# Kernel optimization log

Measured on AMD Instinct MI355X. Metric: run time of the kernel, lower is better.

## Reference

```python
import jax, jax.numpy as jnp
import numpy as np
from jax.scipy.special import logsumexp

D = 256            # descriptor_dim == output_dim
H = 4              # attention heads (hard-coded in AttentionalGNN)
DH = D // H        # 64 per-head dim
KNN = 20           # k for dynamic kNN graph
N_LAYERS = 18      # ['self','cross'] * 9
SINKHORN_ITERS = 20
MATCH_THRESHOLD = 0.2
BN_EPS = 1e-5
N_KPTS = 1024
B = 1
KENC_CH = [D + 4, D // 4, D // 2, D, 2 * D, D]


def conv1(x, w, b):
    # kernel-size-1 Conv1d: x [B,Cin,N], w [Cout,Cin], b [Cout]
    return jnp.einsum('oc,bcn->bon', w, x) + b[:, None]


def bn(x, g, be):
    # training-mode BatchNorm1d over (batch, length), biased variance
    m = jnp.mean(x, axis=(0, 2), keepdims=True)
    v = jnp.var(x, axis=(0, 2), keepdims=True)
    return g[:, None] * (x - m) * jax.lax.rsqrt(v + BN_EPS) + be[:, None]


def run_kenc(desc, kpts, sc, ws, bs, gs, bes):
    # desc [B,N,D], kpts [B,N,3], sc [B,N] -> [B,D,N]
    x = jnp.concatenate([jnp.swapaxes(desc, 1, 2), jnp.swapaxes(kpts, 1, 2), sc[:, None, :]], axis=1)
    for i in range(4):
        x = jax.nn.relu(bn(conv1(x, ws[i], bs[i]), gs[i], bes[i]))
    return conv1(x, ws[4], bs[4])


def run_chebconv(x, pos, cw, cb):
    # x [1,D,N], pos [1,N,3]; dynamic kNN graph + ChebConv K=3, aggr='add'
    p = pos[0]
    n = p.shape[0]
    g = p @ p.T
    sq = jnp.diagonal(g)
    d = sq[:, None] + sq[None, :] - 2.0 * g           # squared pairwise dist [N,N]
    d = d.at[jnp.arange(n), jnp.arange(n)].set(jnp.inf)  # no self-loops
    _, nbr = jax.lax.top_k(-d, KNN)                   # [N,KNN] neighbor indices
    src = jnp.repeat(jnp.arange(n), KNN)              # query node of each edge
    dst = nbr.reshape(-1)                             # neighbor (message target)
    h = x[0].T                                        # [N,D]
    def prop(t):
        # scaled Laplacian propagation: L_hat edge weight = -1/k (self-loops cancel)
        return jnp.zeros_like(t).at[dst].add(t[src]) * (-1.0 / KNN)
    tx0 = h
    tx1 = prop(tx0)
    tx2 = 2.0 * prop(tx1) - tx0
    out = tx0 @ cw[0].T + tx1 @ cw[1].T + tx2 @ cw[2].T + cb
    return out.T[None]                                # [1,D,N]


def attn_prop(x, src, pw, pb, mw, mb, m1w, m1b, g, be, m2w, m2b):
    # AttentionalPropagation: MHA(x, src, src) then MLP([2D,2D,D]) on concat
    b, _, n = x.shape
    m = src.shape[2]
    q = conv1(x, pw[0], pb[0]).reshape(b, DH, H, n)
    k = conv1(src, pw[1], pb[1]).reshape(b, DH, H, m)
    v = conv1(src, pw[2], pb[2]).reshape(b, DH, H, m)
    scores = jnp.einsum('bdhn,bdhm->bhnm', q, k) / (DH ** 0.5)
    prob = jax.nn.softmax(scores, axis=-1)
    msg = jnp.einsum('bhnm,bdhm->bdhn', prob, v).reshape(b, D, n)
    msg = conv1(msg, mw, mb)
    y = jnp.concatenate([x, msg], axis=1)
    y = jax.nn.relu(bn(conv1(y, m1w, m1b), g, be))
    return conv1(y, m2w, m2b)


def log_optimal_transport(scores, alpha, iters):
    b, m, n = scores.shape
    bins0 = jnp.broadcast_to(alpha, (b, m, 1)).astype(scores.dtype)
    bins1 = jnp.broadcast_to(alpha, (b, 1, n)).astype(scores.dtype)
    binsa = jnp.broadcast_to(alpha, (b, 1, 1)).astype(scores.dtype)
    Z = jnp.concatenate([jnp.concatenate([scores, bins0], 2), jnp.concatenate([bins1, binsa], 2)], 1)
    norm = -np.log(float(m + n))
    log_mu = jnp.concatenate([jnp.full((m,), norm, scores.dtype), jnp.asarray([np.log(float(n)) + norm], scores.dtype)])
    log_nu = jnp.concatenate([jnp.full((n,), norm, scores.dtype), jnp.asarray([np.log(float(m)) + norm], scores.dtype)])
    log_mu = jnp.broadcast_to(log_mu[None], (b, m + 1))
    log_nu = jnp.broadcast_to(log_nu[None], (b, n + 1))
    def step(uv, _):
        u, v = uv
        u = log_mu - logsumexp(Z + v[:, None, :], axis=2)
        v = log_nu - logsumexp(Z + u[:, :, None], axis=1)
        return (u, v), None
    (u, v), _ = jax.lax.scan(step, (jnp.zeros_like(log_mu), jnp.zeros_like(log_nu)), None, length=iters)
    return Z + u[:, :, None] + v[:, None, :] - norm


def _forward(h1, h2, uc1, uc2, sc1, sc2, kws, kbs, kgs, kbes, cheb_w, cheb_b,
             gpw, gpb, gmw, gmb, g1w, g1b, gg, gbe, g2w, g2b, fp_w, fp_b, bin_score):
    d1 = run_kenc(h1, uc1, sc1, kws, kbs, kgs, kbes)
    d2 = run_kenc(h2, uc2, sc2, kws, kbs, kgs, kbes)
    d1 = run_chebconv(d1, uc1, cheb_w, cheb_b)
    d2 = run_chebconv(d2, uc2, cheb_w, cheb_b)
    for i in range(N_LAYERS):
        cross = (i % 2 == 1)
        s0, s1 = (d2, d1) if cross else (d1, d2)
        la = (gpw[i], gpb[i], gmw[i], gmb[i], g1w[i], g1b[i], gg[i], gbe[i], g2w[i], g2b[i])
        delta0 = attn_prop(d1, s0, *la)
        delta1 = attn_prop(d2, s1, *la)
        d1, d2 = d1 + delta0, d2 + delta1
    md1 = conv1(d1, fp_w, fp_b)
    md2 = conv1(d2, fp_w, fp_b)
    sc = jnp.einsum('bdn,bdm->bnm', md1, md2) / (D ** 0.5)
    Z = log_optimal_transport(sc, bin_score, SINKHORN_ITERS)
    return Z, md1, md2


def setup_inputs() -> dict:
    key = jax.random.key(0)
    ks = iter(jax.random.split(key, 64))
    def rn(shape, scale=1.0):
        return jax.random.normal(next(ks), shape, dtype=jnp.float32) * scale
    inp = {}
    inp['h1'] = rn((B, N_KPTS, D))
    inp['h2'] = rn((B, N_KPTS, D))
    for nm in ('unitCartesian1', 'unitCartesian2'):
        p = rn((B, N_KPTS, 3))
        inp[nm] = p / jnp.linalg.norm(p, axis=-1, keepdims=True)
    inp['scores1'] = jax.random.uniform(next(ks), (B, N_KPTS), dtype=jnp.float32)
    inp['scores2'] = jax.random.uniform(next(ks), (B, N_KPTS), dtype=jnp.float32)
    for i in range(5):
        ci, co = KENC_CH[i], KENC_CH[i + 1]
        inp['kenc_w%d' % i] = rn((co, ci), ci ** -0.5)
        inp['kenc_b%d' % i] = jnp.zeros((co,), jnp.float32)
    for i in range(4):
        co = KENC_CH[i + 1]
        inp['kenc_g%d' % i] = jnp.ones((co,), jnp.float32)
        inp['kenc_be%d' % i] = jnp.zeros((co,), jnp.float32)
    inp['cheb_w'] = rn((3, D, D), D ** -0.5)
    inp['cheb_b'] = jnp.zeros((D,), jnp.float32)
    L = N_LAYERS
    inp['gnn_proj_w'] = rn((L, 3, D, D), D ** -0.5)
    inp['gnn_proj_b'] = jnp.zeros((L, 3, D), jnp.float32)
    inp['gnn_merge_w'] = rn((L, D, D), D ** -0.5)
    inp['gnn_merge_b'] = jnp.zeros((L, D), jnp.float32)
    inp['gnn_m1_w'] = rn((L, 2 * D, 2 * D), (2 * D) ** -0.5)
    inp['gnn_m1_b'] = jnp.zeros((L, 2 * D), jnp.float32)
    inp['gnn_g'] = jnp.ones((L, 2 * D), jnp.float32)
    inp['gnn_be'] = jnp.zeros((L, 2 * D), jnp.float32)
    inp['gnn_m2_w'] = rn((L, D, 2 * D), (2 * D) ** -0.5)
    inp['gnn_m2_b'] = jnp.zeros((L, D), jnp.float32)
    inp['fp_w'] = rn((D, D), D ** -0.5)
    inp['fp_b'] = jnp.zeros((D,), jnp.float32)
    inp['bin_score'] = jnp.asarray(1.0, jnp.float32)
    return inp


def reference(h1, h2, unitCartesian1, unitCartesian2, scores1, scores2,
              kenc_w0, kenc_b0, kenc_w1, kenc_b1, kenc_w2, kenc_b2, kenc_w3, kenc_b3, kenc_w4, kenc_b4,
              kenc_g0, kenc_be0, kenc_g1, kenc_be1, kenc_g2, kenc_be2, kenc_g3, kenc_be3,
              cheb_w, cheb_b, gnn_proj_w, gnn_proj_b, gnn_merge_w, gnn_merge_b,
              gnn_m1_w, gnn_m1_b, gnn_g, gnn_be, gnn_m2_w, gnn_m2_b, fp_w, fp_b, bin_score):
    kws = [kenc_w0, kenc_w1, kenc_w2, kenc_w3, kenc_w4]
    kbs = [kenc_b0, kenc_b1, kenc_b2, kenc_b3, kenc_b4]
    kgs = [kenc_g0, kenc_g1, kenc_g2, kenc_g3]
    kbes = [kenc_be0, kenc_be1, kenc_be2, kenc_be3]
    Z, md1, md2 = _forward(h1, h2, unitCartesian1, unitCartesian2, scores1, scores2,
                           kws, kbs, kgs, kbes, cheb_w, cheb_b,
                           gnn_proj_w, gnn_proj_b, gnn_merge_w, gnn_merge_b,
                           gnn_m1_w, gnn_m1_b, gnn_g, gnn_be, gnn_m2_w, gnn_m2_b,
                           fp_w, fp_b, bin_score)
    s = Z[:, :-1, :-1]
    max1v = jnp.max(s, axis=2)
    idx1 = jnp.argmax(s, axis=2)
    idx2 = jnp.argmax(s, axis=1)
    mutual = jnp.arange(s.shape[1])[None, :] == jnp.take_along_axis(idx2, idx1, axis=1)
    mscores = jnp.where(mutual, jnp.exp(max1v), jnp.zeros((), s.dtype))
    valid = mutual & (mscores > MATCH_THRESHOLD)
    matches = jnp.where(valid, idx1, -1).astype(jnp.int32)
    return Z, matches, mscores, md1, md2
```

## Files before the change

### kernel.cpp

```cpp
#include <hip/hip_runtime.h>
#include <math.h>

#define NORM_F  ((float)(-7.6246189861593984953))
#define BIN_F   ((float)(-0.6931471805599453094))

__device__ __forceinline__ float exp_cr(float x) { return (float)exp((double)x); }
__device__ __forceinline__ float log_cr(float x) { return (float)log((double)x); }

struct GJob {
  const float* A0; const float* X0;
  const float* A1; const float* X1;
  const float* A2; const float* X2;
  const float* bias; float* C;
  const float* resid;
};
struct GArgs { GJob j[8]; };

struct TJob { const float* A; const float* B; float* C; int cb; };
struct TArgs { TJob j[8]; };

struct VJob { const float* V; const float* P; float* C; };
struct VArgs { VJob j[8]; };

struct NJob { const float* A; const float* B; float* C; };
struct NArgs { NJob j[2]; };

#define MICRO_FMA(w4, x4)                                   \
  acc[0][0] = fmaf(w4.x, x4.x, acc[0][0]);                  \
  acc[0][1] = fmaf(w4.x, x4.y, acc[0][1]);                  \
  acc[0][2] = fmaf(w4.x, x4.z, acc[0][2]);                  \
  acc[0][3] = fmaf(w4.x, x4.w, acc[0][3]);                  \
  acc[1][0] = fmaf(w4.y, x4.x, acc[1][0]);                  \
  acc[1][1] = fmaf(w4.y, x4.y, acc[1][1]);                  \
  acc[1][2] = fmaf(w4.y, x4.z, acc[1][2]);                  \
  acc[1][3] = fmaf(w4.y, x4.w, acc[1][3]);                  \
  acc[2][0] = fmaf(w4.z, x4.x, acc[2][0]);                  \
  acc[2][1] = fmaf(w4.z, x4.y, acc[2][1]);                  \
  acc[2][2] = fmaf(w4.z, x4.z, acc[2][2]);                  \
  acc[2][3] = fmaf(w4.z, x4.w, acc[2][3]);                  \
  acc[3][0] = fmaf(w4.w, x4.x, acc[3][0]);                  \
  acc[3][1] = fmaf(w4.w, x4.y, acc[3][1]);                  \
  acc[3][2] = fmaf(w4.w, x4.z, acc[3][2]);                  \
  acc[3][3] = fmaf(w4.w, x4.w, acc[3][3]);

__global__ __launch_bounds__(256) void concat_kenc(
    const float* __restrict__ h1, const float* __restrict__ h2,
    const float* __restrict__ uc1, const float* __restrict__ uc2,
    const float* __restrict__ s1, const float* __restrict__ s2,
    float* __restrict__ out) {
  int img = blockIdx.y;
  const float* h  = img ? h2 : h1;
  const float* uc = img ? uc2 : uc1;
  const float* sc = img ? s2 : s1;
  float* o = out + (size_t)img * 260 * 1024;
  int idx = blockIdx.x * 256 + threadIdx.x;
  if (idx >= 260 * 1024) return;
  int c = idx >> 10, n = idx & 1023;
  float v;
  if (c < 256)      v = h[(size_t)n * 256 + c];
  else if (c < 259) v = uc[(size_t)n * 3 + (c - 256)];
  else              v = sc[n];
  o[idx] = v;
}

__global__ __launch_bounds__(512) void gemm_std(GArgs args, int nseg, int split,
                                                int ci0, int ci1, int ci2,
                                                int lda, int co) {
  __shared__ float Wt[32][36];
  __shared__ float Xs[32][68];
  GJob jb = args.j[blockIdx.z];
  const int n0 = blockIdx.x * 64;
  const int c0 = blockIdx.y * 32;
  const int t = threadIdx.x, tx = t & 15, ty = t >> 4;
  float acc[4] = {};
  float accT[4] = {};
  const float* As[3] = { jb.A0, jb.A1, jb.A2 };
  const float* Xp[3] = { jb.X0, jb.X1, jb.X2 };
  int cis[3] = { ci0, ci1, ci2 };
  for (int s = 0; s < nseg; ++s) {
    const float* A = As[s];
    const float* X = Xp[s];
    const int ci = cis[s];
    if (split) {
      #pragma unroll
      for (int jj = 0; jj < 4; ++jj) acc[jj] = 0.f;
    }
    for (int k0 = 0; k0 < ci; k0 += 32) {
      if (t < 256) {
        const int row = t >> 3;
        const int kk = (t & 7) * 4;
        const float* srcp = A + (size_t)(c0 + row) * lda + k0 + kk;
        float4 w4;
        if (k0 + kk + 4 <= ci) {
          w4 = *(const float4*)srcp;
        } else {
          w4.x = (k0 + kk + 0 < ci) ? srcp[0] : 0.f;
          w4.y = (k0 + kk + 1 < ci) ? srcp[1] : 0.f;
          w4.z = (k0 + kk + 2 < ci) ? srcp[2] : 0.f;
          w4.w = (k0 + kk + 3 < ci) ? srcp[3] : 0.f;
        }
        Wt[kk + 0][row] = w4.x; Wt[kk + 1][row] = w4.y;
        Wt[kk + 2][row] = w4.z; Wt[kk + 3][row] = w4.w;
      }
      {
        const int kk = t >> 4, nl = (t & 15) * 4;
        float4 x4 = make_float4(0.f, 0.f, 0.f, 0.f);
        if (k0 + kk < ci) x4 = *(const float4*)(X + (size_t)(k0 + kk) * 1024 + n0 + nl);
        *(float4*)&Xs[kk][nl] = x4;
      }
      __syncthreads();
      #pragma unroll
      for (int kk = 0; kk < 32; ++kk) {
        const float w0 = Wt[kk][ty];
        const float4 x4 = *(const float4*)&Xs[kk][tx * 4];
        acc[0] = fmaf(w0, x4.x, acc[0]);
        acc[1] = fmaf(w0, x4.y, acc[1]);
        acc[2] = fmaf(w0, x4.z, acc[2]);
        acc[3] = fmaf(w0, x4.w, acc[3]);
      }
      __syncthreads();
    }
    if (split) {
      #pragma unroll
      for (int jj = 0; jj < 4; ++jj)
        accT[jj] = __fadd_rn(accT[jj], acc[jj]);
    }
  }
  {
    const int row = c0 + ty;
    const float b = jb.bias ? jb.bias[row] : 0.f;
    const float* src = split ? accT : acc;
    float4 o;
    o.x = __fadd_rn(src[0], b); o.y = __fadd_rn(src[1], b);
    o.z = __fadd_rn(src[2], b); o.w = __fadd_rn(src[3], b);
    if (jb.resid) {
      const float4 r4 = *(const float4*)(jb.resid + (size_t)row * 1024 + n0 + tx * 4);
      o.x = __fadd_rn(r4.x, o.x); o.y = __fadd_rn(r4.y, o.y);
      o.z = __fadd_rn(r4.z, o.z); o.w = __fadd_rn(r4.w, o.w);
    }
    *(float4*)(jb.C + (size_t)row * 1024 + n0 + tx * 4) = o;
  }
}

__global__ __launch_bounds__(256) void gemm_tn(TArgs args, int K, int cs,
                                               float scale, int ldc) {
  __shared__ float As[64][68];
  __shared__ float Bs[64][68];
  TJob jb = args.j[blockIdx.z];
  const int m0 = blockIdx.x * 64;
  const int n0 = blockIdx.y * 64;
  const int t = threadIdx.x, tx = t & 15, ty = t >> 4;
  float acc[4][4] = {};
  for (int k0 = 0; k0 < K; k0 += 64) {
    #pragma unroll
    for (int q = 0; q < 4; ++q) {
      const int kk = (t >> 4) + q * 16;
      const int col = (t & 15) * 4;
      const size_t rb = (size_t)(jb.cb + (k0 + kk) * cs) * 1024;
      *(float4*)&As[kk][col] = *(const float4*)(jb.A + rb + n0 + col);
      *(float4*)&Bs[kk][col] = *(const float4*)(jb.B + rb + m0 + col);
    }
    __syncthreads();
    #pragma unroll 16
    for (int kk = 0; kk < 64; ++kk) {
      const float4 w4 = *(const float4*)&As[kk][ty * 4];
      const float4 x4 = *(const float4*)&Bs[kk][tx * 4];
      MICRO_FMA(w4, x4)
    }
    __syncthreads();
  }
  #pragma unroll
  for (int i = 0; i < 4; ++i) {
    float4 o;
    o.x = __fmul_rn(acc[i][0], scale); o.y = __fmul_rn(acc[i][1], scale);
    o.z = __fmul_rn(acc[i][2], scale); o.w = __fmul_rn(acc[i][3], scale);
    *(float4*)(jb.C + (size_t)(n0 + ty * 4 + i) * ldc + m0 + tx * 4) = o;
  }
}

__global__ __launch_bounds__(128) void gemm_vp(VArgs args) {
  __shared__ float Vs[64][36];
  __shared__ float Ps[64][68];
  VJob jb = args.j[blockIdx.z];
  const int n0 = blockIdx.x * 64;
  const int d0 = blockIdx.y * 32;
  const int t = threadIdx.x, tx = t & 15, ty = t >> 4;
  float acc[4][4] = {};
  for (int m0 = 0; m0 < 1024; m0 += 64) {
    #pragma unroll
    for (int q = 0; q < 4; ++q) {
      const int idx = t + q * 128;
      const int d = idx >> 4, m4 = (idx & 15) * 4;
      float4 v4 = *(const float4*)(jb.V + (size_t)(d0 + d) * 4096 + m0 + m4);
      Vs[m4 + 0][d] = v4.x; Vs[m4 + 1][d] = v4.y;
      Vs[m4 + 2][d] = v4.z; Vs[m4 + 3][d] = v4.w;
    }
    #pragma unroll
    for (int q = 0; q < 8; ++q) {
      const int idx = t + q * 128;
      const int n = idx >> 4, m4 = (idx & 15) * 4;
      float4 p4 = *(const float4*)(jb.P + (size_t)(n0 + n) * 1024 + m0 + m4);
      Ps[m4 + 0][n] = p4.x; Ps[m4 + 1][n] = p4.y;
      Ps[m4 + 2][n] = p4.z; Ps[m4 + 3][n] = p4.w;
    }
    __syncthreads();
    #pragma unroll
    for (int mm = 0; mm < 64; ++mm) {
      const float4 w4 = *(const float4*)&Vs[mm][ty * 4];
      const float4 x4 = *(const float4*)&Ps[mm][tx * 4];
      MICRO_FMA(w4, x4)
    }
    __syncthreads();
  }
  #pragma unroll
  for (int i = 0; i < 4; ++i) {
    float4 o;
    o.x = acc[i][0]; o.y = acc[i][1]; o.z = acc[i][2]; o.w = acc[i][3];
    *(float4*)(jb.C + (size_t)(d0 + ty * 4 + i) * 4096 + n0 + tx * 4) = o;
  }
}

__global__ __launch_bounds__(128) void gemm_nt(NArgs args, float scale) {
  __shared__ float Cs[64][36];
  __shared__ float Ds[64][68];
  NJob jb = args.j[blockIdx.z];
  const int d0 = blockIdx.x * 64;
  const int c0 = blockIdx.y * 32;
  const int t = threadIdx.x, tx = t & 15, ty = t >> 4;
  float acc[4][4] = {};
  for (int s0 = 0; s0 < 1024; s0 += 64) {
    #pragma unroll
    for (int q = 0; q < 4; ++q) {
      const int idx = t + q * 128;
      const int c = idx >> 4, s4 = (idx & 15) * 4;
      float4 a4 = *(const float4*)(jb.A + (size_t)(c0 + c) * 1024 + s0 + s4);
      Cs[s4 + 0][c] = a4.x; Cs[s4 + 1][c] = a4.y;
      Cs[s4 + 2][c] = a4.z; Cs[s4 + 3][c] = a4.w;
    }
    #pragma unroll
    for (int q = 0; q < 8; ++q) {
      const int idx = t + q * 128;
      const int d = idx >> 4, s4 = (idx & 15) * 4;
      float4 b4 = *(const float4*)(jb.B + (size_t)(d0 + d) * 1024 + s0 + s4);
      Ds[s4 + 0][d] = b4.x; Ds[s4 + 1][d] = b4.y;
      Ds[s4 + 2][d] = b4.z; Ds[s4 + 3][d] = b4.w;
    }
    __syncthreads();
    #pragma unroll
    for (int ss = 0; ss < 64; ++ss) {
      const float4 w4 = *(const float4*)&Cs[ss][ty * 4];
      const float4 x4 = *(const float4*)&Ds[ss][tx * 4];
      MICRO_FMA(w4, x4)
    }
    __syncthreads();
  }
  #pragma unroll
  for (int i = 0; i < 4; ++i) {
    float4 o;
    o.x = __fmul_rn(acc[i][0], scale); o.y = __fmul_rn(acc[i][1], scale);
    o.z = __fmul_rn(acc[i][2], scale); o.w = __fmul_rn(acc[i][3], scale);
    *(float4*)(jb.C + (size_t)(c0 + ty * 4 + i) * 1024 + d0 + tx * 4) = o;
  }
}

__global__ __launch_bounds__(64) void scatter_adj(const int* __restrict__ nbr,
                                                  float* __restrict__ adj) {
  const int i = blockIdx.x, img = blockIdx.y;
  const int t = threadIdx.x;
  if (t >= 20) return;
  const int dst = nbr[((size_t)img * 1024 + i) * 20 + t];
  adj[(size_t)img * 1048576 + (size_t)dst * 1024 + i] = 1.0f;
}

__global__ __launch_bounds__(256) void bn_relu_par(float* __restrict__ x,
                                                   const float* __restrict__ g,
                                                   const float* __restrict__ be,
                                                   int co) {
  const int ch = blockIdx.x, img = blockIdx.y;
  float* p = x + ((size_t)img * co + ch) * 1024;
  __shared__ float ls[1024];
  __shared__ float sh[2];
  const int t = threadIdx.x;
  #pragma unroll
  for (int q = 0; q < 4; ++q) ls[t + q * 256] = p[t + q * 256];
  __syncthreads();
  if (t < 64) {
    float s = 0.f;
    for (int n = 0; n < 1024; ++n) s = __fadd_rn(s, ls[n]);
    const float mean = __fdiv_rn(s, 1024.f);
    float vs = 0.f;
    for (int n = 0; n < 1024; ++n) {
      const float d = __fsub_rn(ls[n], mean);
      vs = __fadd_rn(vs, __fmul_rn(d, d));
    }
    const float var = __fdiv_rn(vs, 1024.f);
    if (t == 0) {
      sh[0] = mean;
      sh[1] = __fdiv_rn(1.f, sqrtf(__fadd_rn(var, 1e-5f)));
    }
  }
  __syncthreads();
  const float mean = sh[0], rs = sh[1];
  const float gc = g[ch], bc = be[ch];
  #pragma unroll
  for (int q = 0; q < 4; ++q) {
    const int n = t + q * 256;
    float v = __fmul_rn(gc, __fsub_rn(ls[n], mean));
    v = __fmul_rn(v, rs);
    v = __fadd_rn(v, bc);
    p[n] = fmaxf(v, 0.f);
  }
}

__global__ __launch_bounds__(256) void knn_kernel(const float* __restrict__ uc1,
                                                  const float* __restrict__ uc2,
                                                  int* __restrict__ nbr) {
  const int i = blockIdx.x, img = blockIdx.y;
  const float* uc = img ? uc2 : uc1;
  __shared__ float dist[1024];
  __shared__ float rv[256];
  __shared__ int   ri[256];
  const int t = threadIdx.x;
  const float pix = uc[i * 3], piy = uc[i * 3 + 1], piz = uc[i * 3 + 2];
  const float sqi = fmaf(piz, piz, fmaf(piy, piy, __fmul_rn(pix, pix)));
  for (int j = t; j < 1024; j += 256) {
    const float x = uc[j * 3], y = uc[j * 3 + 1], z = uc[j * 3 + 2];
    const float gg  = fmaf(piz, z, fmaf(piy, y, __fmul_rn(pix, x)));
    const float sqj = fmaf(z, z, fmaf(y, y, __fmul_rn(x, x)));
    const float d = __fsub_rn(__fadd_rn(sqi, sqj), __fmul_rn(2.f, gg));
    dist[j] = (j == i) ? INFINITY : d;
  }
  __syncthreads();
  int* out = nbr + ((size_t)img * 1024 + i) * 20;
  for (int k = 0; k < 20; ++k) {
    float bv = INFINITY; int bi = 0x7fffffff;
    for (int j = t; j < 1024; j += 256) {
      const float d = dist[j];
      if (d < bv) { bv = d; bi = j; }
    }
    rv[t] = bv; ri[t] = bi;
    __syncthreads();
    for (int st = 128; st > 0; st >>= 1) {
      if (t < st) {
        const float v2 = rv[t + st]; const int i2 = ri[t + st];
        if (v2 < rv[t] || (v2 == rv[t] && i2 < ri[t])) { rv[t] = v2; ri[t] = i2; }
      }
      __syncthreads();
    }
    if (t == 0) { out[k] = ri[0]; dist[ri[0]] = INFINITY; }
    __syncthreads();
  }
}

__global__ __launch_bounds__(256) void axpby(const float* __restrict__ x,
                                             const float* __restrict__ y,
                                             float* __restrict__ o,
                                             float a, float b, int n) {
  const int i = blockIdx.x * 256 + threadIdx.x;
  if (i < n) o[i] = __fadd_rn(__fmul_rn(a, x[i]), __fmul_rn(b, y[i]));
}

__global__ __launch_bounds__(256) void softmax_par(float* __restrict__ P) {
  float* p = P + (size_t)blockIdx.x * 1024;
  __shared__ float ls[1024];
  __shared__ float red[256];
  const int t = threadIdx.x;
  float mx = -INFINITY;
  #pragma unroll
  for (int q = 0; q < 4; ++q) {
    const float v = p[t + q * 256];
    ls[t + q * 256] = v;
    mx = fmaxf(mx, v);
  }
  red[t] = mx;
  __syncthreads();
  for (int st = 128; st > 0; st >>= 1) { if (t < st) red[t] = fmaxf(red[t], red[t + st]); __syncthreads(); }
  mx = red[0];
  __syncthreads();
  #pragma unroll
  for (int q = 0; q < 4; ++q) {
    const int n = t + q * 256;
    ls[n] = exp_cr(__fsub_rn(ls[n], mx));
  }
  __syncthreads();
  if (t < 64) {
    float s = 0.f;
    for (int n = 0; n < 1024; ++n) s = __fadd_rn(s, ls[n]);
    if (t == 0) red[0] = s;
  }
  __syncthreads();
  const float s = red[0];
  #pragma unroll
  for (int q = 0; q < 4; ++q) {
    const int n = t + q * 256;
    p[n] = __fdiv_rn(ls[n], s);
  }
}

__global__ __launch_bounds__(256) void build_Z(const float* __restrict__ sc,
                                               const float* __restrict__ alpha,
                                               float* __restrict__ Z,
                                               float* __restrict__ ZT) {
  const int idx = blockIdx.x * 256 + threadIdx.x;
  if (idx >= 1025 * 1025) return;
  const int i = idx / 1025, j = idx - i * 1025;
  const float v = (i < 1024 && j < 1024) ? sc[(size_t)i * 1024 + j] : alpha[0];
  Z[idx] = v;
  ZT[(size_t)j * 1025 + i] = v;
}

__global__ __launch_bounds__(256) void lse_par(const float* __restrict__ M,
                                               const float* __restrict__ add,
                                               float* __restrict__ out) {
  const int r = blockIdx.x;
  const float* p = M + (size_t)r * 1025;
  __shared__ float ls[1025];
  __shared__ float red[256];
  const int t = threadIdx.x;
  float mx = -INFINITY;
  for (int j = t; j < 1025; j += 256) {
    const float v = __fadd_rn(p[j], add[j]);
    ls[j] = v;
    mx = fmaxf(mx, v);
  }
  red[t] = mx;
  __syncthreads();
  for (int st = 128; st > 0; st >>= 1) { if (t < st) red[t] = fmaxf(red[t], red[t + st]); __syncthreads(); }
  mx = red[0];
  __syncthreads();
  for (int j = t; j < 1025; j += 256) ls[j] = exp_cr(__fsub_rn(ls[j], mx));
  __syncthreads();
  if (t < 64) {
    float s = 0.f;
    for (int j = 0; j < 1025; ++j) s = __fadd_rn(s, ls[j]);
    if (t == 0) {
      const float logw = (r < 1024) ? NORM_F : BIN_F;
      out[r] = __fsub_rn(logw, __fadd_rn(log_cr(s), mx));
    }
  }
}

__global__ __launch_bounds__(256) void write_final(const float* __restrict__ Z,
                                                   const float* __restrict__ u,
                                                   const float* __restrict__ v,
                                                   float* __restrict__ outZ,
                                                   float* __restrict__ FZc) {
  const int idx = blockIdx.x * 256 + threadIdx.x;
  if (idx >= 1025 * 1025) return;
  const int i = idx / 1025, j = idx - i * 1025;
  float t = __fadd_rn(Z[idx], u[i]);
  t = __fadd_rn(t, v[j]);
  t = __fsub_rn(t, NORM_F);
  outZ[idx] = t;
  FZc[(size_t)j * 1025 + i] = t;
}

__global__ __launch_bounds__(256) void argmax_par(const float* __restrict__ M,
                                                  float* __restrict__ maxout,
                                                  int* __restrict__ idxout) {
  const int r = blockIdx.x;
  const float* p = M + (size_t)r * 1025;
  __shared__ float rv[256];
  __shared__ int   ri[256];
  const int t = threadIdx.x;
  float bv = -INFINITY; int bi = 0x7fffffff;
  for (int j = t; j < 1024; j += 256) {
    const float v = p[j];
    if (v > bv) { bv = v; bi = j; }
  }
  rv[t] = bv; ri[t] = bi;
  __syncthreads();
  for (int st = 128; st > 0; st >>= 1) {
    if (t < st) {
      const float v2 = rv[t + st]; const int i2 = ri[t + st];
      if (v2 > rv[t] || (v2 == rv[t] && i2 < ri[t])) { rv[t] = v2; ri[t] = i2; }
    }
    __syncthreads();
  }
  if (t == 0) {
    idxout[r] = ri[0];
    if (maxout) maxout[r] = rv[0];
  }
}

__global__ __launch_bounds__(256) void matches_kernel(const int* __restrict__ idx1,
                                                      const int* __restrict__ idx2,
                                                      const float* __restrict__ rowmax,
                                                      float* __restrict__ m_out,
                                                      float* __restrict__ s_out) {
  const int i = blockIdx.x * 256 + threadIdx.x;
  if (i >= 1024) return;
  const int j = idx1[i];
  const bool mutual = (idx2[j] == i);
  const float msc = mutual ? exp_cr(rowmax[i]) : 0.f;
  s_out[i] = msc;
  m_out[i] = (mutual && msc > 0.2f) ? (float)j : -1.f;
}

extern "C" void kernel_launch(void* const* d_in, const int* in_sizes, int n_in,
                              void* d_out, int out_size, void* d_ws, size_t ws_size,
                              hipStream_t stream) {
  const float* h1  = (const float*)d_in[0];
  const float* h2  = (const float*)d_in[1];
  const float* uc1 = (const float*)d_in[2];
  const float* uc2 = (const float*)d_in[3];
  const float* s1  = (const float*)d_in[4];
  const float* s2  = (const float*)d_in[5];
  const float* kw[5]  = { (const float*)d_in[6],  (const float*)d_in[8],
                          (const float*)d_in[10], (const float*)d_in[12],
                          (const float*)d_in[14] };
  const float* kb[5]  = { (const float*)d_in[7],  (const float*)d_in[9],
                          (const float*)d_in[11], (const float*)d_in[13],
                          (const float*)d_in[15] };
  const float* kg[4]  = { (const float*)d_in[16], (const float*)d_in[18],
                          (const float*)d_in[20], (const float*)d_in[22] };
  const float* kbe[4] = { (const float*)d_in[17], (const float*)d_in[19],
                          (const float*)d_in[21], (const float*)d_in[23] };
  const float* cheb_w = (const float*)d_in[24];
  const float* cheb_b = (const float*)d_in[25];
  const float* pw = (const float*)d_in[26];
  const float* pb = (const float*)d_in[27];
  const float* mw = (const float*)d_in[28];
  const float* mb = (const float*)d_in[29];
  const float* m1w = (const float*)d_in[30];
  const float* m1b = (const float*)d_in[31];
  const float* gg  = (const float*)d_in[32];
  const float* gbe = (const float*)d_in[33];
  const float* m2w = (const float*)d_in[34];
  const float* m2b = (const float*)d_in[35];
  const float* fpw = (const float*)d_in[36];
  const float* fpb = (const float*)d_in[37];
  const float* bin = (const float*)d_in[38];

  float* ws = (float*)d_ws;
  float* A0   = ws;
  float* A1   = ws + 1048576;
  float* Dm   = ws + 2097152;
  float* DT   = ws + 2621440;
  float* TX1  = ws + 3145728;
  float* TX2  = ws + 3670016;
  float* QKV  = ws + 4194304;
  float* PROB = ws + 5767168;
  float* ADJ = PROB;
  float* SCp = PROB;
  float* Zb  = ws;
  float* ZTb = ws + 1050628;
  float* FZc = ws + 3151884;
  float* Ub  = ws + 4202512;
  float* Vb  = ws + 4203540;
  float* RM  = ws + 4204568;
  int*   I1  = (int*)(ws + 4205592);
  int*   I2  = (int*)(ws + 4206616);
  int*   KNNI = (int*)QKV;
  float* MSG   = A1;
  float* T1    = A0;
  float* outF  = (float*)d_out;
  float* outZ  = outF;
  float* outM  = outF + 1050625;
  float* outS  = outF + 1051649;
  float* outMD1 = outF + 1052673;
  float* outMD2 = outF + 1314817;
  (void)ws_size; (void)in_sizes; (void)n_in; (void)out_size;

  concat_kenc<<<dim3(1040, 2), 256, 0, stream>>>(h1, h2, uc1, uc2, s1, s2, A0);

  const int kci[5] = { 260, 64, 128, 256, 512 };
  const int kco[5] = { 64, 128, 256, 512, 256 };
  float* ping = A0; float* pong = A1;
  for (int L = 0; L < 5; ++L) {
    const int ci = kci[L], co = kco[L];
    float* dst = (L == 4) ? DT : pong;
    GArgs ga = {};
    for (int img = 0; img < 2; ++img) {
      ga.j[img].A0 = kw[L];
      ga.j[img].X0 = ping + (size_t)img * ci * 1024;
      ga.j[img].bias = kb[L];
      ga.j[img].C = dst + (size_t)img * co * 1024;
    }
    gemm_std<<<dim3(16, co / 32, 2), 512, 0, stream>>>(ga, 1, 0, ci, 0, 0, ci, co);
    if (L < 4)
      bn_relu_par<<<dim3(co, 2), 256, 0, stream>>>(dst, kg[L], kbe[L], co);
    float* tmp = ping; ping = pong; pong = tmp;
  }

  knn_kernel<<<dim3(1024, 2), 256, 0, stream>>>(uc1, uc2, KNNI);
  hipMemsetAsync(ADJ, 0, 2u * 1048576u * sizeof(float), stream);
  scatter_adj<<<dim3(1024, 2), 64, 0, stream>>>(KNNI, ADJ);

  {
    NArgs na = {};
    for (int img = 0; img < 2; ++img) {
      na.j[img].A = DT + (size_t)img * 262144;
      na.j[img].B = ADJ + (size_t)img * 1048576;
      na.j[img].C = TX1 + (size_t)img * 262144;
    }
    gemm_nt<<<dim3(16, 8, 2), 128, 0, stream>>>(na, -0.05f);
  }
  {
    NArgs na = {};
    for (int img = 0; img < 2; ++img) {
      na.j[img].A = TX1 + (size_t)img * 262144;
      na.j[img].B = ADJ + (size_t)img * 1048576;
      na.j[img].C = A0 + (size_t)img * 262144;
    }
    gemm_nt<<<dim3(16, 8, 2), 128, 0, stream>>>(na, -0.05f);
  }
  axpby<<<2048, 256, 0, stream>>>(A0, DT, TX2, 2.f, -1.f, 524288);

  {
    GArgs ga = {};
    for (int img = 0; img < 2; ++img) {
      ga.j[img].A0 = cheb_w;           ga.j[img].X0 = DT  + (size_t)img * 262144;
      ga.j[img].A1 = cheb_w + 65536;   ga.j[img].X1 = TX1 + (size_t)img * 262144;
      ga.j[img].A2 = cheb_w + 131072;  ga.j[img].X2 = TX2 + (size_t)img * 262144;
      ga.j[img].bias = cheb_b;
      ga.j[img].C = Dm + (size_t)img * 262144;
    }
    gemm_std<<<dim3(16, 8, 2), 512, 0, stream>>>(ga, 3, 1, 256, 256, 256, 256, 256);
  }

  float* qb = QKV;
  float* kb_ = QKV + 524288;
  float* vb = QKV + 1048576;
  float* MSG2 = QKV;
  for (int l = 0; l < 18; ++l) {
    const int cross = l & 1;
    const float* x[2]   = { Dm, Dm + 262144 };
    const float* src[2] = { cross ? x[1] : x[0], cross ? x[0] : x[1] };

    {
      GArgs ga = {};
      for (int p = 0; p < 3; ++p)
        for (int img = 0; img < 2; ++img) {
          GJob& j = ga.j[p * 2 + img];
          j.A0 = pw + ((size_t)(l * 3 + p)) * 65536;
          j.X0 = (p == 0) ? x[img] : src[img];
          j.bias = pb + ((size_t)(l * 3 + p)) * 256;
          j.C = QKV + ((size_t)(p * 2 + img)) * 262144;
        }
      gemm_std<<<dim3(16, 8, 6), 512, 0, stream>>>(ga, 1, 0, 256, 0, 0, 256, 256);
    }
    {
      TArgs ta = {};
      for (int img = 0; img < 2; ++img)
        for (int h = 0; h < 4; ++h) {
          TJob& j = ta.j[img * 4 + h];
          j.A = qb + (size_t)img * 262144;
          j.B = kb_ + (size_t)img * 262144;
          j.C = PROB + ((size_t)(img * 4 + h)) * 1048576;
          j.cb = h;
        }
      gemm_tn<<<dim3(16, 16, 8), 256, 0, stream>>>(ta, 64, 4, 0.125f, 1024);
    }
    softmax_par<<<8192, 256, 0, stream>>>(PROB);
    {
      VArgs va = {};
      for (int img = 0; img < 2; ++img)
        for (int h = 0; h < 4; ++h) {
          VJob& j = va.j[img * 4 + h];
          j.V = vb + (size_t)img * 262144 + h * 1024;
          j.P = PROB + ((size_t)(img * 4 + h)) * 1048576;
          j.C = MSG + (size_t)img * 262144 + h * 1024;
        }
      gemm_vp<<<dim3(16, 2, 8), 128, 0, stream>>>(va);
    }
    {
      GArgs ga = {};
      for (int img = 0; img < 2; ++img) {
        ga.j[img].A0 = mw + (size_t)l * 65536;
        ga.j[img].X0 = MSG + (size_t)img * 262144;
        ga.j[img].bias = mb + (size_t)l * 256;
        ga.j[img].C = MSG2 + (size_t)img * 262144;
      }
      gemm_std<<<dim3(16, 8, 2), 512, 0, stream>>>(ga, 1, 0, 256, 0, 0, 256, 256);
    }
    {
      GArgs ga = {};
      for (int img = 0; img < 2; ++img) {
        ga.j[img].A0 = m1w + (size_t)l * 262144;        ga.j[img].X0 = x[img];
        ga.j[img].A1 = m1w + (size_t)l * 262144 + 256;  ga.j[img].X1 = MSG2 + (size_t)img * 262144;
        ga.j[img].bias = m1b + (size_t)l * 512;
        ga.j[img].C = T1 + (size_t)img * 524288;
      }
      gemm_std<<<dim3(16, 16, 2), 512, 0, stream>>>(ga, 2, 0, 256, 256, 0, 512, 512);
    }
    bn_relu_par<<<dim3(512, 2), 256, 0, stream>>>(T1, gg + (size_t)l * 512, gbe + (size_t)l * 512, 512);
    {
      GArgs ga = {};
      for (int img = 0; img < 2; ++img) {
        ga.j[img].A0 = m2w + (size_t)l * 131072;
        ga.j[img].X0 = T1 + (size_t)img * 524288;
        ga.j[img].bias = m2b + (size_t)l * 256;
        ga.j[img].C = Dm + (size_t)img * 262144;
        ga.j[img].resid = Dm + (size_t)img * 262144;
      }
      gemm_std<<<dim3(16, 8, 2), 512, 0, stream>>>(ga, 1, 0, 512, 0, 0, 512, 256);
    }
  }

  {
    GArgs ga = {};
    for (int img = 0; img < 2; ++img) {
      ga.j[img].A0 = fpw;
      ga.j[img].X0 = Dm + (size_t)img * 262144;
      ga.j[img].bias = fpb;
      ga.j[img].C = (img ? outMD2 : outMD1);
    }
    gemm_std<<<dim3(16, 8, 2), 512, 0, stream>>>(ga, 1, 0, 256, 0, 0, 256, 256);
  }
  {
    TArgs ta = {};
    ta.j[0].A = outMD1; ta.j[0].B = outMD2; ta.j[0].C = SCp; ta.j[0].cb = 0;
    gemm_tn<<<dim3(16, 16, 1), 256, 0, stream>>>(ta, 256, 1, 0.0625f, 1024);
  }

  build_Z<<<4105, 256, 0, stream>>>(SCp, bin, Zb, ZTb);
  hipMemsetAsync(Ub, 0, 1025 * sizeof(float), stream);
  hipMemsetAsync(Vb, 0, 1025 * sizeof(float), stream);
  for (int it = 0; it < 20; ++it) {
    lse_par<<<1025, 256, 0, stream>>>(Zb, Vb, Ub);
    lse_par<<<1025, 256, 0, stream>>>(ZTb, Ub, Vb);
  }
  write_final<<<4105, 256, 0, stream>>>(Zb, Ub, Vb, outZ, FZc);

  argmax_par<<<1024, 256, 0, stream>>>(outZ, RM, I1);
  argmax_par<<<1024, 256, 0, stream>>>(FZc, (float*)nullptr, I2);
  matches_kernel<<<4, 256, 0, stream>>>(I1, I2, RM, outM, outS);
}
```

Baseline: 4.636 ms.

## Fuse QK^T, softmax and PV into a single attention kernel

Replaces the three-kernel attention path (QK^T GEMM writing a 32MB probability buffer, a row softmax kernel, and the PV GEMM) with one kernel. Each block handles 8 query rows of one head and keeps the full score rows in shared memory. This removes the global-memory round trips of the probability matrix and two launches per layer. In exchange the QK and PV products now use scalar 1x2 register tiling instead of 4x4 micro-tiles, and the 34KB+ shared footprint limits occupancy. K and V are re-read from global by every block.

```diff
diff --git a/kernel.cpp b/kernel.cpp
--- a/kernel.cpp
+++ b/kernel.cpp
@@ -18,9 +18,6 @@
 
 struct TJob { const float* A; const float* B; float* C; int cb; };
 struct TArgs { TJob j[8]; };
-
-struct VJob { const float* V; const float* P; float* C; };
-struct VArgs { VJob j[8]; };
 
 struct NJob { const float* A; const float* B; float* C; };
 struct NArgs { NJob j[2]; };
@@ -178,46 +175,109 @@
   }
 }
 
-__global__ __launch_bounds__(128) void gemm_vp(VArgs args) {
-  __shared__ float Vs[64][36];
-  __shared__ float Ps[64][68];
-  VJob jb = args.j[blockIdx.z];
-  const int n0 = blockIdx.x * 64;
-  const int d0 = blockIdx.y * 32;
-  const int t = threadIdx.x, tx = t & 15, ty = t >> 4;
-  float acc[4][4] = {};
-  for (int m0 = 0; m0 < 1024; m0 += 64) {
-    #pragma unroll
-    for (int q = 0; q < 4; ++q) {
-      const int idx = t + q * 128;
-      const int d = idx >> 4, m4 = (idx & 15) * 4;
-      float4 v4 = *(const float4*)(jb.V + (size_t)(d0 + d) * 4096 + m0 + m4);
-      Vs[m4 + 0][d] = v4.x; Vs[m4 + 1][d] = v4.y;
-      Vs[m4 + 2][d] = v4.z; Vs[m4 + 3][d] = v4.w;
-    }
-    #pragma unroll
-    for (int q = 0; q < 8; ++q) {
-      const int idx = t + q * 128;
-      const int n = idx >> 4, m4 = (idx & 15) * 4;
-      float4 p4 = *(const float4*)(jb.P + (size_t)(n0 + n) * 1024 + m0 + m4);
-      Ps[m4 + 0][n] = p4.x; Ps[m4 + 1][n] = p4.y;
-      Ps[m4 + 2][n] = p4.z; Ps[m4 + 3][n] = p4.w;
+__global__ __launch_bounds__(256) void attn_fused(const float* __restrict__ QKVbuf,
+                                                  float* __restrict__ MSGout) {
+  const int n0  = blockIdx.x * 8;
+  const int img = blockIdx.y >> 2;
+  const int h   = blockIdx.y & 3;
+  const float* Q = QKVbuf + (size_t)img * 262144;
+  const float* K = QKVbuf + 524288 + (size_t)img * 262144;
+  const float* V = QKVbuf + 1048576 + (size_t)img * 262144;
+  float* MSG = MSGout + (size_t)img * 262144;
+
+  __shared__ float sc[8 * 1024];
+  __shared__ float kvt[64 * 68];
+  __shared__ float Qs[64 * 8];
+  __shared__ float red[256];
+  __shared__ float mxr[8];
+  __shared__ float ssum[8];
+  const int t = threadIdx.x;
+
+  #pragma unroll
+  for (int q = 0; q < 2; ++q) {
+    const int idx = t + q * 256;
+    const int k = idx >> 3, r = idx & 7;
+    Qs[k * 8 + r] = Q[(size_t)(h + 4 * k) * 1024 + n0 + r];
+  }
+  __syncthreads();
+
+  const int r_a = t >> 5;
+  const int ml  = t & 31;
+  for (int mt = 0; mt < 16; ++mt) {
+    #pragma unroll
+    for (int q = 0; q < 16; ++q) {
+      const int idx = t + q * 256;
+      const int k = idx >> 6, mm = idx & 63;
+      kvt[k * 68 + mm] = K[(size_t)(h + 4 * k) * 1024 + mt * 64 + mm];
+    }
+    __syncthreads();
+    float s0 = 0.f, s1 = 0.f;
+    #pragma unroll
+    for (int k = 0; k < 64; ++k) {
+      const float qv = Qs[k * 8 + r_a];
+      s0 = fmaf(qv, kvt[k * 68 + ml], s0);
+      s1 = fmaf(qv, kvt[k * 68 + ml + 32], s1);
+    }
+    sc[r_a * 1024 + mt * 64 + ml]      = __fmul_rn(s0, 0.125f);
+    sc[r_a * 1024 + mt * 64 + ml + 32] = __fmul_rn(s1, 0.125f);
+    __syncthreads();
+  }
+
+  {
+    float mx = -INFINITY;
+    for (int j = ml; j < 1024; j += 32) mx = fmaxf(mx, sc[r_a * 1024 + j]);
+    red[r_a * 32 + ml] = mx;
+    __syncthreads();
+    for (int st = 16; st > 0; st >>= 1) {
+      if (ml < st) red[r_a * 32 + ml] = fmaxf(red[r_a * 32 + ml], red[r_a * 32 + ml + st]);
+      __syncthreads();
+    }
+    if (t < 8) mxr[t] = red[t * 32];
+    __syncthreads();
+    #pragma unroll
+    for (int q = 0; q < 32; ++q) {
+      const int idx = t + q * 256;
+      const int r = idx >> 10, j = idx & 1023;
+      sc[r * 1024 + j] = exp_cr(__fsub_rn(sc[r * 1024 + j], mxr[r]));
+    }
+    __syncthreads();
+    const int w = t >> 6;
+    for (int rr = w; rr < 8; rr += 4) {
+      float s = 0.f;
+      for (int j = 0; j < 1024; ++j) s = __fadd_rn(s, sc[rr * 1024 + j]);
+      if ((t & 63) == 0) ssum[rr] = s;
+    }
+    __syncthreads();
+    #pragma unroll
+    for (int q = 0; q < 32; ++q) {
+      const int idx = t + q * 256;
+      const int r = idx >> 10, j = idx & 1023;
+      sc[r * 1024 + j] = __fdiv_rn(sc[r * 1024 + j], ssum[r]);
+    }
+    __syncthreads();
+  }
+
+  const int d_c = t & 63;
+  const int r0  = t >> 6;
+  float m0a = 0.f, m1a = 0.f;
+  for (int mt = 0; mt < 16; ++mt) {
+    #pragma unroll
+    for (int q = 0; q < 16; ++q) {
+      const int idx = t + q * 256;
+      const int d = idx >> 6, mm = idx & 63;
+      kvt[mm * 65 + d] = V[(size_t)(h + 4 * d) * 1024 + mt * 64 + mm];
     }
     __syncthreads();
     #pragma unroll
     for (int mm = 0; mm < 64; ++mm) {
-      const float4 w4 = *(const float4*)&Vs[mm][ty * 4];
-      const float4 x4 = *(const float4*)&Ps[mm][tx * 4];
-      MICRO_FMA(w4, x4)
-    }
-    __syncthreads();
-  }
-  #pragma unroll
-  for (int i = 0; i < 4; ++i) {
-    float4 o;
-    o.x = acc[i][0]; o.y = acc[i][1]; o.z = acc[i][2]; o.w = acc[i][3];
-    *(float4*)(jb.C + (size_t)(d0 + ty * 4 + i) * 4096 + n0 + tx * 4) = o;
-  }
+      const float v = kvt[mm * 65 + d_c];
+      m0a = fmaf(sc[r0 * 1024 + mt * 64 + mm], v, m0a);
+      m1a = fmaf(sc[(r0 + 4) * 1024 + mt * 64 + mm], v, m1a);
+    }
+    __syncthreads();
+  }
+  MSG[(size_t)(h + 4 * d_c) * 1024 + n0 + r0]     = m0a;
+  MSG[(size_t)(h + 4 * d_c) * 1024 + n0 + r0 + 4] = m1a;
 }
 
 __global__ __launch_bounds__(128) void gemm_nt(NArgs args, float scale) {
@@ -358,43 +418,6 @@
                                              float a, float b, int n) {
   const int i = blockIdx.x * 256 + threadIdx.x;
   if (i < n) o[i] = __fadd_rn(__fmul_rn(a, x[i]), __fmul_rn(b, y[i]));
-}
-
-__global__ __launch_bounds__(256) void softmax_par(float* __restrict__ P) {
-  float* p = P + (size_t)blockIdx.x * 1024;
-  __shared__ float ls[1024];
-  __shared__ float red[256];
-  const int t = threadIdx.x;
-  float mx = -INFINITY;
-  #pragma unroll
-  for (int q = 0; q < 4; ++q) {
-    const float v = p[t + q * 256];
-    ls[t + q * 256] = v;
-    mx = fmaxf(mx, v);
-  }
-  red[t] = mx;
-  __syncthreads();
-  for (int st = 128; st > 0; st >>= 1) { if (t < st) red[t] = fmaxf(red[t], red[t + st]); __syncthreads(); }
-  mx = red[0];
-  __syncthreads();
-  #pragma unroll
-  for (int q = 0; q < 4; ++q) {
-    const int n = t + q * 256;
-    ls[n] = exp_cr(__fsub_rn(ls[n], mx));
-  }
-  __syncthreads();
-  if (t < 64) {
-    float s = 0.f;
-    for (int n = 0; n < 1024; ++n) s = __fadd_rn(s, ls[n]);
-    if (t == 0) red[0] = s;
-  }
-  __syncthreads();
-  const float s = red[0];
-  #pragma unroll
-  for (int q = 0; q < 4; ++q) {
-    const int n = t + q * 256;
-    p[n] = __fdiv_rn(ls[n], s);
-  }
 }
 
 __global__ __launch_bounds__(256) void build_Z(const float* __restrict__ sc,
@@ -619,9 +642,6 @@
     gemm_std<<<dim3(16, 8, 2), 512, 0, stream>>>(ga, 3, 1, 256, 256, 256, 256, 256);
   }
 
-  float* qb = QKV;
-  float* kb_ = QKV + 524288;
-  float* vb = QKV + 1048576;
   float* MSG2 = QKV;
   for (int l = 0; l < 18; ++l) {
     const int cross = l & 1;
@@ -640,30 +660,7 @@
         }
       gemm_std<<<dim3(16, 8, 6), 512, 0, stream>>>(ga, 1, 0, 256, 0, 0, 256, 256);
     }
-    {
-      TArgs ta = {};
-      for (int img = 0; img < 2; ++img)
-        for (int h = 0; h < 4; ++h) {
-          TJob& j = ta.j[img * 4 + h];
-          j.A = qb + (size_t)img * 262144;
-          j.B = kb_ + (size_t)img * 262144;
-          j.C = PROB + ((size_t)(img * 4 + h)) * 1048576;
-          j.cb = h;
-        }
-      gemm_tn<<<dim3(16, 16, 8), 256, 0, stream>>>(ta, 64, 4, 0.125f, 1024);
-    }
-    softmax_par<<<8192, 256, 0, stream>>>(PROB);
-    {
-      VArgs va = {};
-      for (int img = 0; img < 2; ++img)
-        for (int h = 0; h < 4; ++h) {
-          VJob& j = va.j[img * 4 + h];
-          j.V = vb + (size_t)img * 262144 + h * 1024;
-          j.P = PROB + ((size_t)(img * 4 + h)) * 1048576;
-          j.C = MSG + (size_t)img * 262144 + h * 1024;
-        }
-      gemm_vp<<<dim3(16, 2, 8), 128, 0, stream>>>(va);
-    }
+    attn_fused<<<dim3(128, 8), 256, 0, stream>>>(QKV, MSG);
     {
       GArgs ga = {};
       for (int img = 0; img < 2; ++img) {
```

After: 10.03 ms. 2.16x slower.
